# Performance work log

Measured on AMD Instinct MI355X. Metric: run time of the kernel, lower is better.

Reference implementation:

```python
import jax, jax.numpy as jnp
import numpy as np

N_FR, N_FV, N_REL, N_VAL, N_KN = 512, 512, 256, 256, 512
TOPK_FR, TOPK_FV, TOPK_REL, TOPK_VAL = 8, 8, 4, 6
EPS = 1e-8


def setup_inputs() -> dict:
    key = jax.random.key(0)
    k1, k2, k3, k4 = jax.random.split(key, 4)
    B, S, D, DS = 8, 2048, 2048, 64
    N = N_FR + N_FV + N_REL + N_VAL + N_KN  # 2304
    return {
        "x": jax.random.normal(k1, (B, S, D), dtype=jnp.float32),
        "importance": jax.random.uniform(k2, (B, S), dtype=jnp.float32),
        "W": jax.random.normal(k3, (DS, D), dtype=jnp.float32) * (1.0 / np.sqrt(D)),
        "b": jnp.zeros((DS,), dtype=jnp.float32),
        "neuron_emb": jax.random.normal(k4, (N, DS), dtype=jnp.float32) * 0.02,
    }


def _topk_sparsify(w, k):
    # w: [B, n] -> keep top-k values, zero the rest, renormalize to sum 1
    vals, idx = jax.lax.top_k(w, k)
    B = w.shape[0]
    sparse = jnp.zeros_like(w).at[jnp.arange(B)[:, None], idx].set(vals)
    return sparse / (sparse.sum(axis=-1, keepdims=True) + EPS)


def reference(x, importance, W, b, neuron_emb):
    # Projection (nn.Linear): [B,S,d_space]; dropout is identity in eval mode
    h = jnp.einsum('bsd,kd->bsk', x, W) + b
    # Normalized neuron embeddings (F.normalize along dim=-1)
    emb = neuron_emb / jnp.linalg.norm(neuron_emb, axis=-1, keepdims=True)
    # All routing logits in one shot: [B, S, total_neurons]
    all_logits = jnp.einsum('bsk,nk->bsn', h, emb)

    fr_end = N_FR
    fv_end = N_FR + N_FV
    rel_end = fv_end + N_REL
    val_end = rel_end + N_VAL

    fr_pref = jax.nn.softmax(all_logits[..., :fr_end], axis=-1)
    fv_pref = jax.nn.softmax(all_logits[..., fr_end:fv_end], axis=-1)
    rel_pref = jax.nn.softmax(all_logits[..., fv_end:rel_end], axis=-1)  # shared by Q and K
    val_pref = jax.nn.softmax(all_logits[..., rel_end:val_end], axis=-1)

    def dense(pref):
        return jnp.einsum('bs,bsn->bn', importance, pref)

    fr_w = _topk_sparsify(dense(fr_pref), TOPK_FR)
    fv_w = _topk_sparsify(dense(fv_pref), TOPK_FV)
    rel_d = dense(rel_pref)
    rq_w = _topk_sparsify(rel_d, TOPK_REL)
    rk_w = rq_w  # relational_Q and relational_K slices are identical
    val_w = _topk_sparsify(dense(val_pref), TOPK_VAL)

    # Concatenate the five per-batch routing weight vectors: [B, 512+512+256+256+256]
    return jnp.concatenate([fr_w, fv_w, rq_w, rk_w, val_w], axis=-1)
```

## Files before the change

### kernel.cpp

```cpp
#include <hip/hip_runtime.h>
#include <hip/hip_bf16.h>
#include <hip/hip_fp16.h>

#define B_    8
#define S_    2048
#define D_    2048
#define DS_   64
#define NUSED 1536
#define TOK   16384

typedef __attribute__((ext_vector_type(8))) short bf16x8;
typedef __attribute__((ext_vector_type(4))) float f32x4;

static constexpr int WS_ETF   = 0;
static constexpr int WS_HT    = 98304;
static constexpr int WS_HF    = 2195456;
static constexpr int WS_PART  = 3244032;
static constexpr int WS_PART2 = 4816896;
static constexpr int WS_WF    = 4915200;

typedef __attribute__((address_space(1))) const void g_void;
typedef __attribute__((address_space(3))) void l_void;

__device__ inline short bf_hi(float f, float& rhi) {
    __hip_bfloat16 h = __float2bfloat16(f);
    rhi = __bfloat162float(h);
    return __builtin_bit_cast(short, h);
}
__device__ inline short bf_of(float f) {
    __hip_bfloat16 h = __float2bfloat16(f);
    return __builtin_bit_cast(short, h);
}
__device__ inline int sliceOfTile(int tile) {
    return tile < 32 ? 0 : tile < 64 ? 1 : tile < 80 ? 2 : 3;
}

__launch_bounds__(256)
__global__ void k_wsplit(const float* __restrict__ W, short* __restrict__ wfrag) {
    const int t = threadIdx.x, kstep = blockIdx.x;
    const int msub = t >> 6, lane = t & 63;
    const int m = msub * 16 + (lane & 15);
    const float* wp = W + m * D_ + kstep * 32 + (lane >> 4) * 8;
    float4 a = *reinterpret_cast<const float4*>(wp);
    float4 b = *reinterpret_cast<const float4*>(wp + 4);
    float f[8] = {a.x, a.y, a.z, a.w, b.x, b.y, b.z, b.w};
    bf16x8 hi, lo;
#pragma unroll
    for (int j = 0; j < 8; ++j) {
        float r;
        hi[j] = bf_hi(f[j], r);
        lo[j] = bf_of(f[j] - r);
    }
    short* base = wfrag + (size_t)(kstep * 4 + msub) * 1024;
    *reinterpret_cast<bf16x8*>(base + lane * 8)       = hi;
    *reinterpret_cast<bf16x8*>(base + 512 + lane * 8) = lo;
}

__launch_bounds__(128)
__global__ void k_embpack(const float* __restrict__ emb, short* __restrict__ etfrag) {
    __shared__ float red[16][8];
    __shared__ float rn[16];
    const int tid = threadIdx.x;
    const int kh = tid >> 6, lane = tid & 63;
    const int tile = blockIdx.x;
    const int nl = lane & 15;
    const int n = tile * 16 + nl;
    const int kb = kh * 32 + (lane >> 4) * 8;
    const float* ep = emb + n * DS_ + kb;
    float4 a = *reinterpret_cast<const float4*>(ep);
    float4 b = *reinterpret_cast<const float4*>(ep + 4);
    float f[8] = {a.x, a.y, a.z, a.w, b.x, b.y, b.z, b.w};
    float ss = 0.f;
#pragma unroll
    for (int j = 0; j < 8; ++j) ss += f[j] * f[j];
    red[nl][kh * 4 + (lane >> 4)] = ss;
    __syncthreads();
    if (tid < 16) {
        float s = 0.f;
#pragma unroll
        for (int j = 0; j < 8; ++j) s += red[tid][j];
        rn[tid] = 1.0f / sqrtf(s);
    }
    __syncthreads();
    const float r0 = rn[nl];
    bf16x8 hi, lo;
#pragma unroll
    for (int j = 0; j < 8; ++j) {
        float v = f[j] * r0, r;
        hi[j] = bf_hi(v, r);
        lo[j] = bf_of(v - r);
    }
    short* dst = etfrag + (size_t)((tile * 2 + kh) * 64 + lane) * 16;
    *reinterpret_cast<bf16x8*>(dst)     = hi;
    *reinterpret_cast<bf16x8*>(dst + 8) = lo;
}

#define MFMA16(A, Bv, C) __builtin_amdgcn_mfma_f32_16x16x32_bf16(A, Bv, C, 0, 0, 0)

__launch_bounds__(256, 2)
__global__ void k_gemm1(const float* __restrict__ x, const short* __restrict__ wfrag,
                        float* __restrict__ htp) {
    __shared__ short wlds[2][4096];

    const int tid   = threadIdx.x;
    const int split = blockIdx.x & 1;
    const int tb    = (blockIdx.x >> 1) * 64;
    const int wave  = tid >> 6, lane = tid & 63;
    const int tok   = tb + wave * 16 + (lane & 15);

    const float* xp   = x + (size_t)tok * D_ + split * 1024 + (lane >> 4) * 8;
    const short* wsrc = wfrag + (size_t)(split * 32) * 4096;

    f32x4 acc0 = {0.f, 0.f, 0.f, 0.f};
    f32x4 acc1 = acc0, acc2 = acc0, acc3 = acc0;

    __builtin_amdgcn_global_load_lds((g_void*)(wsrc + tid * 8),
                                     (l_void*)(&wlds[0][tid * 8]), 16, 0, 0);
    __builtin_amdgcn_global_load_lds((g_void*)(wsrc + 2048 + tid * 8),
                                     (l_void*)(&wlds[0][2048 + tid * 8]), 16, 0, 0);
    float4 xa = *reinterpret_cast<const float4*>(xp);
    float4 xb = *reinterpret_cast<const float4*>(xp + 4);

    for (int ks = 0; ks < 32; ++ks) {
        __syncthreads();
        const int buf = ks & 1;
        if (ks < 31) {
            const short* ns = wsrc + (size_t)(ks + 1) * 4096;
            __builtin_amdgcn_global_load_lds((g_void*)(ns + tid * 8),
                                             (l_void*)(&wlds[buf ^ 1][tid * 8]), 16, 0, 0);
            __builtin_amdgcn_global_load_lds((g_void*)(ns + 2048 + tid * 8),
                                             (l_void*)(&wlds[buf ^ 1][2048 + tid * 8]), 16, 0, 0);
        }

        float xf[8] = {xa.x, xa.y, xa.z, xa.w, xb.x, xb.y, xb.z, xb.w};
        bf16x8 bh, bl;
#pragma unroll
        for (int j = 0; j < 8; ++j) {
            float r;
            bh[j] = bf_hi(xf[j], r);
            bl[j] = bf_of(xf[j] - r);
        }
        if (ks < 31) {
            xa = *reinterpret_cast<const float4*>(xp + (ks + 1) * 32);
            xb = *reinterpret_cast<const float4*>(xp + (ks + 1) * 32 + 4);
        }

        const short* wl = &wlds[buf][0];
        bf16x8 ah0 = *reinterpret_cast<const bf16x8*>(wl +    0 + lane * 8);
        bf16x8 al0 = *reinterpret_cast<const bf16x8*>(wl +  512 + lane * 8);
        bf16x8 ah1 = *reinterpret_cast<const bf16x8*>(wl + 1024 + lane * 8);
        bf16x8 al1 = *reinterpret_cast<const bf16x8*>(wl + 1536 + lane * 8);
        bf16x8 ah2 = *reinterpret_cast<const bf16x8*>(wl + 2048 + lane * 8);
        bf16x8 al2 = *reinterpret_cast<const bf16x8*>(wl + 2560 + lane * 8);
        bf16x8 ah3 = *reinterpret_cast<const bf16x8*>(wl + 3072 + lane * 8);
        bf16x8 al3 = *reinterpret_cast<const bf16x8*>(wl + 3584 + lane * 8);

        acc0 = MFMA16(ah0, bh, acc0);
        acc1 = MFMA16(ah1, bh, acc1);
        acc2 = MFMA16(ah2, bh, acc2);
        acc3 = MFMA16(ah3, bh, acc3);
        acc0 = MFMA16(al0, bh, acc0);
        acc1 = MFMA16(al1, bh, acc1);
        acc2 = MFMA16(al2, bh, acc2);
        acc3 = MFMA16(al3, bh, acc3);
        acc0 = MFMA16(ah0, bl, acc0);
        acc1 = MFMA16(ah1, bl, acc1);
        acc2 = MFMA16(ah2, bl, acc2);
        acc3 = MFMA16(ah3, bl, acc3);
    }

    const int row0 = split * 64 + (lane >> 4) * 4;
    const int col  = tb + wave * 16 + (lane & 15);
#pragma unroll
    for (int r = 0; r < 4; ++r) {
        htp[(size_t)(row0 +  0 + r) * TOK + col] = acc0[r];
        htp[(size_t)(row0 + 16 + r) * TOK + col] = acc1[r];
        htp[(size_t)(row0 + 32 + r) * TOK + col] = acc2[r];
        htp[(size_t)(row0 + 48 + r) * TOK + col] = acc3[r];
    }
}

__launch_bounds__(256)
__global__ void k_hfix(const float* __restrict__ htp, const float* __restrict__ bias,
                       short* __restrict__ hfrag) {
    const int idx = blockIdx.x * 256 + threadIdx.x;
    const int tt = idx >> 7, rem = idx & 127;
    const int kh = rem >> 6, lane = rem & 63;
    const int t = tt * 16 + (lane & 15);
    const int kb = kh * 32 + (lane >> 4) * 8;
    bf16x8 hi, lo;
#pragma unroll
    for (int j = 0; j < 8; ++j) {
        const int k = kb + j;
        float v = htp[(size_t)k * TOK + t] + htp[(size_t)(k + 64) * TOK + t] + bias[k];
        float r;
        hi[j] = bf_hi(v, r);
        lo[j] = bf_of(v - r);
    }
    short* dst = hfrag + (size_t)((tt * 2 + kh) * 64 + lane) * 16;
    *reinterpret_cast<bf16x8*>(dst)     = hi;
    *reinterpret_cast<bf16x8*>(dst + 8) = lo;
}

__launch_bounds__(512, 2)
__global__ void k_route2(const short* __restrict__ hfrag, const short* __restrict__ etfrag,
                         const float* __restrict__ imp, float* __restrict__ part) {
    __shared__ float zw[8][2][16];
    __shared__ float coef[4][16];
    __shared__ float impb[16];

    const int tid = threadIdx.x;
    const int w = tid >> 6, lane = tid & 63;
    const int tt = blockIdx.x;
    const int tk = lane & 15, g = lane >> 4;

    const short* hp = hfrag + (size_t)(tt * 2) * 1024 + lane * 16;
    bf16x8 bh0 = *reinterpret_cast<const bf16x8*>(hp);
    bf16x8 bl0 = *reinterpret_cast<const bf16x8*>(hp + 8);
    bf16x8 bh1 = *reinterpret_cast<const bf16x8*>(hp + 1024);
    bf16x8 bl1 = *reinterpret_cast<const bf16x8*>(hp + 1032);

    if (tid < 16) impb[tid] = imp[tt * 16 + tid];

    const int t0 = w * 12;
    const int sA = sliceOfTile(t0);
    const int sB = sliceOfTile(t0 + 11);
    float zacc0 = 0.f, zacc1 = 0.f;
    float p[12][4];

    const short* ep = etfrag + (size_t)t0 * 2048 + lane * 16;
#pragma unroll
    for (int ti = 0; ti < 12; ++ti) {
        const short* cp = ep + (size_t)ti * 2048;
        bf16x8 ah0 = *reinterpret_cast<const bf16x8*>(cp);
        bf16x8 al0 = *reinterpret_cast<const bf16x8*>(cp + 8);
        bf16x8 ah1 = *reinterpret_cast<const bf16x8*>(cp + 1024);
        bf16x8 al1 = *reinterpret_cast<const bf16x8*>(cp + 1032);
        f32x4 a0 = {0.f, 0.f, 0.f, 0.f};
        f32x4 a1 = {0.f, 0.f, 0.f, 0.f};
        a0 = MFMA16(ah0, bh0, a0);
        a1 = MFMA16(ah1, bh1, a1);
        a0 = MFMA16(al0, bh0, a0);
        a1 = MFMA16(al1, bh1, a1);
        a0 = MFMA16(ah0, bl0, a0);
        a1 = MFMA16(ah1, bl1, a1);
        const float p0 = __expf(a0[0] + a1[0]);
        const float p1 = __expf(a0[1] + a1[1]);
        const float p2 = __expf(a0[2] + a1[2]);
        const float p3 = __expf(a0[3] + a1[3]);
        p[ti][0] = p0; p[ti][1] = p1; p[ti][2] = p2; p[ti][3] = p3;
        const float zs = (p0 + p1) + (p2 + p3);
        if (sliceOfTile(t0 + ti) == sA) zacc0 += zs; else zacc1 += zs;
    }

    zacc0 += __shfl_xor(zacc0, 16); zacc0 += __shfl_xor(zacc0, 32);
    zacc1 += __shfl_xor(zacc1, 16); zacc1 += __shfl_xor(zacc1, 32);
    if (lane < 16) { zw[w][0][lane] = zacc0; zw[w][1][lane] = zacc1; }
    __syncthreads();

    if (tid < 64) {
        const int s = tid >> 4, k2 = tid & 15;
        float z = 0.f;
#pragma unroll
        for (int w2 = 0; w2 < 8; ++w2) {
            const int a = sliceOfTile(w2 * 12);
            const int b = sliceOfTile(w2 * 12 + 11);
            if (a == s) z += zw[w2][0][k2];
            if (b == s && b != a) z += zw[w2][1][k2];
        }
        coef[s][k2] = impb[k2] / z;
    }
    __syncthreads();

    const float cA = coef[sA][tk];
    const float cB = coef[sB][tk];
    float* pout = part + (size_t)tt * NUSED;
#pragma unroll
    for (int ti = 0; ti < 12; ++ti) {
        const float c = (sliceOfTile(t0 + ti) == sA) ? cA : cB;
        float v0 = p[ti][0] * c, v1 = p[ti][1] * c, v2 = p[ti][2] * c, v3 = p[ti][3] * c;
#pragma unroll
        for (int st = 1; st < 16; st <<= 1) {
            v0 += __shfl_xor(v0, st);
            v1 += __shfl_xor(v1, st);
            v2 += __shfl_xor(v2, st);
            v3 += __shfl_xor(v3, st);
        }
        if (tk == 0)
            *reinterpret_cast<float4*>(&pout[(t0 + ti) * 16 + g * 4]) =
                make_float4(v0, v1, v2, v3);
    }
}

__launch_bounds__(256)
__global__ void kA(const float* __restrict__ part, float* __restrict__ part2) {
    const int tid = threadIdx.x;
    const int b = blockIdx.x >> 3, g = blockIdx.x & 7;
    const int base = (b * 128 + g * 16) * NUSED;
#pragma unroll
    for (int i = 0; i < 6; ++i) {
        int n = tid + 256 * i;
        float s = 0.f;
#pragma unroll
        for (int r = 0; r < 16; ++r) s += part[base + r * NUSED + n];
        part2[(b * 8 + g) * NUSED + n] = s;
    }
}

__launch_bounds__(256)
__global__ void kB(const float* __restrict__ part2, float* __restrict__ out) {
    __shared__ float dens[NUSED];
    __shared__ float s_v[4][8];
    __shared__ int   s_n[4][8];
    const int tid = threadIdx.x;
    const int b = blockIdx.x;

#pragma unroll
    for (int i = 0; i < 6; ++i) {
        int n = tid + 256 * i;
        float s = 0.f;
#pragma unroll
        for (int g = 0; g < 8; ++g) s += part2[(b * 8 + g) * NUSED + n];
        dens[n] = s;
    }
    for (int i = tid; i < 1792; i += 256) out[b * 1792 + i] = 0.f;
    __syncthreads();

    const int w = tid >> 6, lane = tid & 63;
    const int soffs[4] = {0, 512, 1024, 1280};
    const int ssz[4]   = {512, 512, 256, 256};
    const int kks[4]   = {8, 8, 4, 6};
    const int ooffs[4] = {0, 512, 1024, 1536};
    const int Sn = ssz[w], soff = soffs[w], kk = kks[w];
    const int nslots = Sn >> 6;

    float v[8];
#pragma unroll
    for (int i = 0; i < 8; ++i)
        v[i] = (i < nslots) ? dens[soff + lane + 64 * i] : -1e30f;

    unsigned rm = 0;
    float ssum = 0.f;
    for (int it = 0; it < kk; ++it) {
        float bv = -1e30f;
        int bn = 0x7fffffff;
#pragma unroll
        for (int i = 0; i < 8; ++i) {
            bool valid = (i < nslots) && !((rm >> i) & 1u);
            if (valid && v[i] > bv) { bv = v[i]; bn = lane + 64 * i; }
        }
#pragma unroll
        for (int off = 32; off; off >>= 1) {
            float ov = __shfl_xor(bv, off);
            int   on = __shfl_xor(bn, off);
            if (ov > bv || (ov == bv && on < bn)) { bv = ov; bn = on; }
        }
        ssum += bv;
        if ((bn & 63) == lane) rm |= 1u << (bn >> 6);
        if (lane == 0) { s_v[w][it] = bv; s_n[w][it] = bn; }
    }
    const float inv = 1.f / (ssum + 1e-8f);
    if (lane < kk) {
        int n = s_n[w][lane];
        float val = s_v[w][lane] * inv;
        out[b * 1792 + ooffs[w] + n] = val;
        if (w == 2) out[b * 1792 + 1280 + n] = val;
    }
}

extern "C" void kernel_launch(void* const* d_in, const int* in_sizes, int n_in,
                              void* d_out, int out_size, void* d_ws, size_t ws_size,
                              hipStream_t stream) {
    const float* x    = (const float*)d_in[0];
    const float* imp  = (const float*)d_in[1];
    const float* W    = (const float*)d_in[2];
    const float* bias = (const float*)d_in[3];
    const float* emb  = (const float*)d_in[4];
    float* out = (float*)d_out;
    float* ws  = (float*)d_ws;

    short* etfrag = (short*)(ws + WS_ETF);
    float* htp    = ws + WS_HT;
    short* hfrag  = (short*)(ws + WS_HF);
    float* part   = ws + WS_PART;
    float* part2  = ws + WS_PART2;
    short* wfrag  = (short*)(ws + WS_WF);

    k_embpack<<<96, 128, 0, stream>>>(emb, etfrag);
    k_wsplit<<<64, 256, 0, stream>>>(W, wfrag);
    k_gemm1<<<512, 256, 0, stream>>>(x, wfrag, htp);
    k_hfix<<<512, 256, 0, stream>>>(htp, bias, hfrag);
    k_route2<<<1024, 512, 0, stream>>>(hfrag, etfrag, imp, part);
    kA<<<64, 256, 0, stream>>>(part, part2);
    kB<<<8, 256, 0, stream>>>(part2, out);
}
```

Baseline: 87.42 us.

## Fuse preprocessing kernels, fold hfix into route2, and double k-step staging in gemm1

Merges the embedding-normalize and W-split kernels into one launch, and removes the separate h-fixup kernel: route2 now reads the two split-K partials plus bias directly into LDS and builds the bf16 hi/lo fragments itself. The first GEMM stages two k-steps per LDS buffer, which halves the barrier count and issues larger prefetches. This cuts two kernel launches and one round trip of intermediate data through global memory. In exchange gemm1 uses twice the LDS and more registers, which may lower occupancy.

```diff
diff --git a/kernel.cpp b/kernel.cpp
--- a/kernel.cpp
+++ b/kernel.cpp
@@ -1,6 +1,5 @@
 #include <hip/hip_runtime.h>
 #include <hip/hip_bf16.h>
-#include <hip/hip_fp16.h>
 
 #define B_    8
 #define S_    2048
@@ -12,12 +11,11 @@
 typedef __attribute__((ext_vector_type(8))) short bf16x8;
 typedef __attribute__((ext_vector_type(4))) float f32x4;
 
-static constexpr int WS_ETF   = 0;
-static constexpr int WS_HT    = 98304;
-static constexpr int WS_HF    = 2195456;
-static constexpr int WS_PART  = 3244032;
-static constexpr int WS_PART2 = 4816896;
-static constexpr int WS_WF    = 4915200;
+static constexpr int WS_ETF  = 0;
+static constexpr int WS_HT   = 98304;
+static constexpr int WS_PART = 2195456;
+static constexpr int WS_PART2= 3768320;
+static constexpr int WS_WF   = 3866624;
 
 typedef __attribute__((address_space(1))) const void g_void;
 typedef __attribute__((address_space(3))) void l_void;
@@ -36,63 +34,64 @@
 }
 
 __launch_bounds__(256)
-__global__ void k_wsplit(const float* __restrict__ W, short* __restrict__ wfrag) {
-    const int t = threadIdx.x, kstep = blockIdx.x;
-    const int msub = t >> 6, lane = t & 63;
-    const int m = msub * 16 + (lane & 15);
-    const float* wp = W + m * D_ + kstep * 32 + (lane >> 4) * 8;
-    float4 a = *reinterpret_cast<const float4*>(wp);
-    float4 b = *reinterpret_cast<const float4*>(wp + 4);
-    float f[8] = {a.x, a.y, a.z, a.w, b.x, b.y, b.z, b.w};
-    bf16x8 hi, lo;
-#pragma unroll
-    for (int j = 0; j < 8; ++j) {
-        float r;
-        hi[j] = bf_hi(f[j], r);
-        lo[j] = bf_of(f[j] - r);
-    }
-    short* base = wfrag + (size_t)(kstep * 4 + msub) * 1024;
-    *reinterpret_cast<bf16x8*>(base + lane * 8)       = hi;
-    *reinterpret_cast<bf16x8*>(base + 512 + lane * 8) = lo;
-}
-
-__launch_bounds__(128)
-__global__ void k_embpack(const float* __restrict__ emb, short* __restrict__ etfrag) {
-    __shared__ float red[16][8];
-    __shared__ float rn[16];
+__global__ void k_pre(const float* __restrict__ emb, const float* __restrict__ W,
+                      short* __restrict__ etfrag, short* __restrict__ wfrag) {
+    __shared__ float red[2][16][8];
+    __shared__ float rn[2][16];
     const int tid = threadIdx.x;
-    const int kh = tid >> 6, lane = tid & 63;
-    const int tile = blockIdx.x;
-    const int nl = lane & 15;
-    const int n = tile * 16 + nl;
-    const int kb = kh * 32 + (lane >> 4) * 8;
-    const float* ep = emb + n * DS_ + kb;
-    float4 a = *reinterpret_cast<const float4*>(ep);
-    float4 b = *reinterpret_cast<const float4*>(ep + 4);
-    float f[8] = {a.x, a.y, a.z, a.w, b.x, b.y, b.z, b.w};
-    float ss = 0.f;
-#pragma unroll
-    for (int j = 0; j < 8; ++j) ss += f[j] * f[j];
-    red[nl][kh * 4 + (lane >> 4)] = ss;
-    __syncthreads();
-    if (tid < 16) {
-        float s = 0.f;
-#pragma unroll
-        for (int j = 0; j < 8; ++j) s += red[tid][j];
-        rn[tid] = 1.0f / sqrtf(s);
-    }
-    __syncthreads();
-    const float r0 = rn[nl];
-    bf16x8 hi, lo;
-#pragma unroll
-    for (int j = 0; j < 8; ++j) {
-        float v = f[j] * r0, r;
-        hi[j] = bf_hi(v, r);
-        lo[j] = bf_of(v - r);
-    }
-    short* dst = etfrag + (size_t)((tile * 2 + kh) * 64 + lane) * 16;
-    *reinterpret_cast<bf16x8*>(dst)     = hi;
-    *reinterpret_cast<bf16x8*>(dst + 8) = lo;
+    if (blockIdx.x < 48) {
+        const int tl = tid >> 7, tid2 = tid & 127;
+        const int kh = tid2 >> 6, lane = tid2 & 63;
+        const int tile = blockIdx.x * 2 + tl;
+        const int nl = lane & 15;
+        const int n = tile * 16 + nl;
+        const int kb = kh * 32 + (lane >> 4) * 8;
+        const float* ep = emb + n * DS_ + kb;
+        float4 a = *reinterpret_cast<const float4*>(ep);
+        float4 b = *reinterpret_cast<const float4*>(ep + 4);
+        float f[8] = {a.x, a.y, a.z, a.w, b.x, b.y, b.z, b.w};
+        float ss = 0.f;
+#pragma unroll
+        for (int j = 0; j < 8; ++j) ss += f[j] * f[j];
+        red[tl][nl][kh * 4 + (lane >> 4)] = ss;
+        __syncthreads();
+        if (tid2 < 16) {
+            float s = 0.f;
+#pragma unroll
+            for (int j = 0; j < 8; ++j) s += red[tl][tid2][j];
+            rn[tl][tid2] = 1.0f / sqrtf(s);
+        }
+        __syncthreads();
+        const float r0 = rn[tl][nl];
+        bf16x8 hi, lo;
+#pragma unroll
+        for (int j = 0; j < 8; ++j) {
+            float v = f[j] * r0, r;
+            hi[j] = bf_hi(v, r);
+            lo[j] = bf_of(v - r);
+        }
+        short* dst = etfrag + (size_t)((tile * 2 + kh) * 64 + lane) * 16;
+        *reinterpret_cast<bf16x8*>(dst)     = hi;
+        *reinterpret_cast<bf16x8*>(dst + 8) = lo;
+    } else {
+        const int kstep = blockIdx.x - 48;
+        const int msub = tid >> 6, lane = tid & 63;
+        const int m = msub * 16 + (lane & 15);
+        const float* wp = W + m * D_ + kstep * 32 + (lane >> 4) * 8;
+        float4 a = *reinterpret_cast<const float4*>(wp);
+        float4 b = *reinterpret_cast<const float4*>(wp + 4);
+        float f[8] = {a.x, a.y, a.z, a.w, b.x, b.y, b.z, b.w};
+        bf16x8 hi, lo;
+#pragma unroll
+        for (int j = 0; j < 8; ++j) {
+            float r;
+            hi[j] = bf_hi(f[j], r);
+            lo[j] = bf_of(f[j] - r);
+        }
+        short* base = wfrag + (size_t)(kstep * 4 + msub) * 1024;
+        *reinterpret_cast<bf16x8*>(base + lane * 8)       = hi;
+        *reinterpret_cast<bf16x8*>(base + 512 + lane * 8) = lo;
+    }
 }
 
 #define MFMA16(A, Bv, C) __builtin_amdgcn_mfma_f32_16x16x32_bf16(A, Bv, C, 0, 0, 0)
@@ -100,7 +99,7 @@
 __launch_bounds__(256, 2)
 __global__ void k_gemm1(const float* __restrict__ x, const short* __restrict__ wfrag,
                         float* __restrict__ htp) {
-    __shared__ short wlds[2][4096];
+    __shared__ short wlds[2][2][4096];
 
     const int tid   = threadIdx.x;
     const int split = blockIdx.x & 1;
@@ -114,59 +113,74 @@
     f32x4 acc0 = {0.f, 0.f, 0.f, 0.f};
     f32x4 acc1 = acc0, acc2 = acc0, acc3 = acc0;
 
-    __builtin_amdgcn_global_load_lds((g_void*)(wsrc + tid * 8),
-                                     (l_void*)(&wlds[0][tid * 8]), 16, 0, 0);
-    __builtin_amdgcn_global_load_lds((g_void*)(wsrc + 2048 + tid * 8),
-                                     (l_void*)(&wlds[0][2048 + tid * 8]), 16, 0, 0);
-    float4 xa = *reinterpret_cast<const float4*>(xp);
-    float4 xb = *reinterpret_cast<const float4*>(xp + 4);
-
-    for (int ks = 0; ks < 32; ++ks) {
+#define STAGE(g, buf)                                                                        \
+    {                                                                                        \
+        const short* s0 = wsrc + (size_t)(2 * (g)) * 4096;                                   \
+        __builtin_amdgcn_global_load_lds((g_void*)(s0 + tid * 8),                            \
+                                         (l_void*)(&wlds[buf][0][tid * 8]), 16, 0, 0);       \
+        __builtin_amdgcn_global_load_lds((g_void*)(s0 + 2048 + tid * 8),                     \
+                                         (l_void*)(&wlds[buf][0][2048 + tid * 8]), 16, 0, 0);\
+        __builtin_amdgcn_global_load_lds((g_void*)(s0 + 4096 + tid * 8),                     \
+                                         (l_void*)(&wlds[buf][1][tid * 8]), 16, 0, 0);       \
+        __builtin_amdgcn_global_load_lds((g_void*)(s0 + 6144 + tid * 8),                     \
+                                         (l_void*)(&wlds[buf][1][2048 + tid * 8]), 16, 0, 0);\
+    }
+
+    STAGE(0, 0);
+    float4 xc0 = *reinterpret_cast<const float4*>(xp);
+    float4 xc1 = *reinterpret_cast<const float4*>(xp + 4);
+    float4 xc2 = *reinterpret_cast<const float4*>(xp + 32);
+    float4 xc3 = *reinterpret_cast<const float4*>(xp + 36);
+
+#pragma unroll 2
+    for (int g = 0; g < 16; ++g) {
         __syncthreads();
-        const int buf = ks & 1;
-        if (ks < 31) {
-            const short* ns = wsrc + (size_t)(ks + 1) * 4096;
-            __builtin_amdgcn_global_load_lds((g_void*)(ns + tid * 8),
-                                             (l_void*)(&wlds[buf ^ 1][tid * 8]), 16, 0, 0);
-            __builtin_amdgcn_global_load_lds((g_void*)(ns + 2048 + tid * 8),
-                                             (l_void*)(&wlds[buf ^ 1][2048 + tid * 8]), 16, 0, 0);
-        }
-
-        float xf[8] = {xa.x, xa.y, xa.z, xa.w, xb.x, xb.y, xb.z, xb.w};
-        bf16x8 bh, bl;
-#pragma unroll
-        for (int j = 0; j < 8; ++j) {
-            float r;
-            bh[j] = bf_hi(xf[j], r);
-            bl[j] = bf_of(xf[j] - r);
-        }
-        if (ks < 31) {
-            xa = *reinterpret_cast<const float4*>(xp + (ks + 1) * 32);
-            xb = *reinterpret_cast<const float4*>(xp + (ks + 1) * 32 + 4);
-        }
-
-        const short* wl = &wlds[buf][0];
-        bf16x8 ah0 = *reinterpret_cast<const bf16x8*>(wl +    0 + lane * 8);
-        bf16x8 al0 = *reinterpret_cast<const bf16x8*>(wl +  512 + lane * 8);
-        bf16x8 ah1 = *reinterpret_cast<const bf16x8*>(wl + 1024 + lane * 8);
-        bf16x8 al1 = *reinterpret_cast<const bf16x8*>(wl + 1536 + lane * 8);
-        bf16x8 ah2 = *reinterpret_cast<const bf16x8*>(wl + 2048 + lane * 8);
-        bf16x8 al2 = *reinterpret_cast<const bf16x8*>(wl + 2560 + lane * 8);
-        bf16x8 ah3 = *reinterpret_cast<const bf16x8*>(wl + 3072 + lane * 8);
-        bf16x8 al3 = *reinterpret_cast<const bf16x8*>(wl + 3584 + lane * 8);
-
-        acc0 = MFMA16(ah0, bh, acc0);
-        acc1 = MFMA16(ah1, bh, acc1);
-        acc2 = MFMA16(ah2, bh, acc2);
-        acc3 = MFMA16(ah3, bh, acc3);
-        acc0 = MFMA16(al0, bh, acc0);
-        acc1 = MFMA16(al1, bh, acc1);
-        acc2 = MFMA16(al2, bh, acc2);
-        acc3 = MFMA16(al3, bh, acc3);
-        acc0 = MFMA16(ah0, bl, acc0);
-        acc1 = MFMA16(ah1, bl, acc1);
-        acc2 = MFMA16(ah2, bl, acc2);
-        acc3 = MFMA16(ah3, bl, acc3);
+        const int buf = g & 1;
+        float4 xn0, xn1, xn2, xn3;
+        if (g < 15) {
+            STAGE(g + 1, buf ^ 1);
+            const float* nxp = xp + (size_t)(g + 1) * 64;
+            xn0 = *reinterpret_cast<const float4*>(nxp);
+            xn1 = *reinterpret_cast<const float4*>(nxp + 4);
+            xn2 = *reinterpret_cast<const float4*>(nxp + 32);
+            xn3 = *reinterpret_cast<const float4*>(nxp + 36);
+        }
+#pragma unroll
+        for (int kk = 0; kk < 2; ++kk) {
+            const float4 va = kk ? xc2 : xc0;
+            const float4 vb = kk ? xc3 : xc1;
+            float xf[8] = {va.x, va.y, va.z, va.w, vb.x, vb.y, vb.z, vb.w};
+            bf16x8 bh, bl;
+#pragma unroll
+            for (int j = 0; j < 8; ++j) {
+                float r;
+                bh[j] = bf_hi(xf[j], r);
+                bl[j] = bf_of(xf[j] - r);
+            }
+            const short* wl = &wlds[buf][kk][0];
+            bf16x8 ah0 = *reinterpret_cast<const bf16x8*>(wl +    0 + lane * 8);
+            bf16x8 al0 = *reinterpret_cast<const bf16x8*>(wl +  512 + lane * 8);
+            bf16x8 ah1 = *reinterpret_cast<const bf16x8*>(wl + 1024 + lane * 8);
+            bf16x8 al1 = *reinterpret_cast<const bf16x8*>(wl + 1536 + lane * 8);
+            bf16x8 ah2 = *reinterpret_cast<const bf16x8*>(wl + 2048 + lane * 8);
+            bf16x8 al2 = *reinterpret_cast<const bf16x8*>(wl + 2560 + lane * 8);
+            bf16x8 ah3 = *reinterpret_cast<const bf16x8*>(wl + 3072 + lane * 8);
+            bf16x8 al3 = *reinterpret_cast<const bf16x8*>(wl + 3584 + lane * 8);
+
+            acc0 = MFMA16(ah0, bh, acc0);
+            acc1 = MFMA16(ah1, bh, acc1);
+            acc2 = MFMA16(ah2, bh, acc2);
+            acc3 = MFMA16(ah3, bh, acc3);
+            acc0 = MFMA16(al0, bh, acc0);
+            acc1 = MFMA16(al1, bh, acc1);
+            acc2 = MFMA16(al2, bh, acc2);
+            acc3 = MFMA16(al3, bh, acc3);
+            acc0 = MFMA16(ah0, bl, acc0);
+            acc1 = MFMA16(ah1, bl, acc1);
+            acc2 = MFMA16(ah2, bl, acc2);
+            acc3 = MFMA16(ah3, bl, acc3);
+        }
+        if (g < 15) { xc0 = xn0; xc1 = xn1; xc2 = xn2; xc3 = xn3; }
     }
 
     const int row0 = split * 64 + (lane >> 4) * 4;
@@ -180,31 +194,11 @@
     }
 }
 
-__launch_bounds__(256)
-__global__ void k_hfix(const float* __restrict__ htp, const float* __restrict__ bias,
-                       short* __restrict__ hfrag) {
-    const int idx = blockIdx.x * 256 + threadIdx.x;
-    const int tt = idx >> 7, rem = idx & 127;
-    const int kh = rem >> 6, lane = rem & 63;
-    const int t = tt * 16 + (lane & 15);
-    const int kb = kh * 32 + (lane >> 4) * 8;
-    bf16x8 hi, lo;
-#pragma unroll
-    for (int j = 0; j < 8; ++j) {
-        const int k = kb + j;
-        float v = htp[(size_t)k * TOK + t] + htp[(size_t)(k + 64) * TOK + t] + bias[k];
-        float r;
-        hi[j] = bf_hi(v, r);
-        lo[j] = bf_of(v - r);
-    }
-    short* dst = hfrag + (size_t)((tt * 2 + kh) * 64 + lane) * 16;
-    *reinterpret_cast<bf16x8*>(dst)     = hi;
-    *reinterpret_cast<bf16x8*>(dst + 8) = lo;
-}
-
 __launch_bounds__(512, 2)
-__global__ void k_route2(const short* __restrict__ hfrag, const short* __restrict__ etfrag,
-                         const float* __restrict__ imp, float* __restrict__ part) {
+__global__ void k_route2(const float* __restrict__ htp, const float* __restrict__ bias,
+                         const short* __restrict__ etfrag, const float* __restrict__ imp,
+                         float* __restrict__ part) {
+    __shared__ float h_lds[64][16];
     __shared__ float zw[8][2][16];
     __shared__ float coef[4][16];
     __shared__ float impb[16];
@@ -214,13 +208,34 @@
     const int tt = blockIdx.x;
     const int tk = lane & 15, g = lane >> 4;
 
-    const short* hp = hfrag + (size_t)(tt * 2) * 1024 + lane * 16;
-    bf16x8 bh0 = *reinterpret_cast<const bf16x8*>(hp);
-    bf16x8 bl0 = *reinterpret_cast<const bf16x8*>(hp + 8);
-    bf16x8 bh1 = *reinterpret_cast<const bf16x8*>(hp + 1024);
-    bf16x8 bl1 = *reinterpret_cast<const bf16x8*>(hp + 1032);
-
+    if (tid < 256) {
+        const int k = tid >> 2, t4 = (tid & 3) << 2;
+        const float4* hp4 = reinterpret_cast<const float4*>(htp);
+        const int col = tt * 4 + (tid & 3);
+        float4 a = hp4[(size_t)k * 4096 + col];
+        float4 b = hp4[(size_t)(k + 64) * 4096 + col];
+        float bk = bias[k];
+        float4 s;
+        s.x = a.x + b.x + bk;
+        s.y = a.y + b.y + bk;
+        s.z = a.z + b.z + bk;
+        s.w = a.w + b.w + bk;
+        *reinterpret_cast<float4*>(&h_lds[k][t4]) = s;
+    }
     if (tid < 16) impb[tid] = imp[tt * 16 + tid];
+    __syncthreads();
+
+    bf16x8 bh0, bl0, bh1, bl1;
+#pragma unroll
+    for (int j = 0; j < 8; ++j) {
+        float r;
+        float v0 = h_lds[g * 8 + j][tk];
+        bh0[j] = bf_hi(v0, r);
+        bl0[j] = bf_of(v0 - r);
+        float v1 = h_lds[32 + g * 8 + j][tk];
+        bh1[j] = bf_hi(v1, r);
+        bl1[j] = bf_of(v1 - r);
+    }
 
     const int t0 = w * 12;
     const int sA = sliceOfTile(t0);
@@ -381,16 +396,13 @@
 
     short* etfrag = (short*)(ws + WS_ETF);
     float* htp    = ws + WS_HT;
-    short* hfrag  = (short*)(ws + WS_HF);
     float* part   = ws + WS_PART;
     float* part2  = ws + WS_PART2;
     short* wfrag  = (short*)(ws + WS_WF);
 
-    k_embpack<<<96, 128, 0, stream>>>(emb, etfrag);
-    k_wsplit<<<64, 256, 0, stream>>>(W, wfrag);
+    k_pre<<<112, 256, 0, stream>>>(emb, W, etfrag, wfrag);
     k_gemm1<<<512, 256, 0, stream>>>(x, wfrag, htp);
-    k_hfix<<<512, 256, 0, stream>>>(htp, bias, hfrag);
-    k_route2<<<1024, 512, 0, stream>>>(hfrag, etfrag, imp, part);
+    k_route2<<<1024, 512, 0, stream>>>(htp, bias, etfrag, imp, part);
     kA<<<64, 256, 0, stream>>>(part, part2);
     kB<<<8, 256, 0, stream>>>(part2, out);
 }
```

Result: faster. 77.42 us (-11.4%).
